# Optimization experiments

Hardware: AMD Instinct MI355X
Metric: run time of the kernel (lower is better)

Reference implementation:

```python
import jax, jax.numpy as jnp
import numpy as np
import math

B = 524288
D = 4
CTX = 64
HID = 128
IN_DIM = 2 + CTX  # keep_idx len is 2 for every mask
# default_masks_D(4, 10) dedups to exactly these 4 masks (torch module therefore has 4 layers)
KEEP = ((0, 1), (1, 2), (2, 3), (0, 3))
TRANS = ((2, 3), (0, 3), (0, 1), (1, 2))
L = 4


def _mlp(x, W1, b1, W2, b2, W3, b3):
    # MLP(in_dim, out_dim, hidden=128, depth=2): Lin+GELU, Lin+GELU, Lin
    x = jax.nn.gelu(x @ W1 + b1, approximate=False)
    x = jax.nn.gelu(x @ W2 + b2, approximate=False)
    return x @ W3 + b3


def setup_inputs() -> dict:
    key = jax.random.key(0)
    ks = jax.random.split(key, 16)
    theta = jax.random.normal(ks[0], (B, D), dtype=jnp.float32)
    h = jax.random.normal(ks[1], (B, CTX), dtype=jnp.float32)
    p = lambda k, shape: jax.random.normal(k, shape, dtype=jnp.float32) * 0.02
    inp = {"theta": theta, "h": h}
    # stacked per-layer weights for s_net and t_net
    for pref, off in (("s", 2), ("t", 8)):
        inp[pref + "W1"] = p(ks[off + 0], (L, IN_DIM, HID))
        inp[pref + "b1"] = p(ks[off + 1], (L, HID))
        inp[pref + "W2"] = p(ks[off + 2], (L, HID, HID))
        inp[pref + "b2"] = p(ks[off + 3], (L, HID))
        inp[pref + "W3"] = p(ks[off + 4], (L, HID, 2))
        inp[pref + "b3"] = p(ks[off + 5], (L, 2))
    return inp


def reference(theta, h, sW1, sb1, sW2, sb2, sW3, sb3, tW1, tb1, tW2, tb2, tW3, tb3):
    # ConditionalRealNVP.log_prob(theta, h)
    x = theta
    logdet = jnp.zeros(theta.shape[0], dtype=theta.dtype)
    for i in range(L):
        keep = np.array(KEEP[i])
        trans = np.array(TRANS[i])
        xp = jnp.concatenate([x[:, keep], h], axis=1)  # [B, 66]
        s = _mlp(xp, sW1[i], sb1[i], sW2[i], sb2[i], sW3[i], sb3[i])  # [B, 2]
        t = _mlp(xp, tW1[i], tb1[i], tW2[i], tb2[i], tW3[i], tb3[i])  # [B, 2]
        x = x.at[:, trans].set(x[:, trans] * jnp.exp(s) + t)
        logdet = logdet + s.sum(axis=1)
    log_pz = -0.5 * (x ** 2).sum(axis=1) - 0.5 * D * math.log(2 * math.pi)
    return log_pz + logdet
```

## Files before the change

kernel.cpp:

```cpp
#include <hip/hip_runtime.h>
#include <hip/hip_bf16.h>

typedef short short8 __attribute__((ext_vector_type(8)));
typedef float f32x4 __attribute__((ext_vector_type(4)));
typedef float f32x2 __attribute__((ext_vector_type(2)));
typedef unsigned short u16;
typedef unsigned int u32;
typedef u32 u32x4 __attribute__((ext_vector_type(4)));

#define NL_STRIDE 57344
#define OFF_W1F 0
#define OFF_W2F 16384
#define OFF_W3F 49152
#define OFF_W1K 53248
#define OFF_B1  54272
#define OFF_B2  54784
#define OFF_B3  55296

__device__ __forceinline__ u16 f2bf(float f) {
  union { float f; unsigned int u; } v; v.f = f;
  unsigned int r = v.u + 0x7fffu + ((v.u >> 16) & 1u);
  return (u16)(r >> 16);
}

__device__ __forceinline__ u32 cvt_pk_bf16(float lo, float hi) {
  u32 r;
  asm("v_cvt_pk_bf16_f32 %0, %1, %2" : "=v"(r) : "v"(lo), "v"(hi));
  return r;
}

__device__ __forceinline__ f32x2 bc2(float s) { return (f32x2){s, s}; }

__device__ __forceinline__ f32x2 gelu2(f32x2 x) {
  f32x2 u = x * x;
  f32x2 t = u * 0.00417617f + (-0.0560330f);
  t = t * u + 0.394326f;
  f32x2 s = x * t + 0.5f;
  s.x = __builtin_amdgcn_fmed3f(s.x, 0.0f, 1.0f);
  s.y = __builtin_amdgcn_fmed3f(s.y, 0.0f, 1.0f);
  return x * s;
}

__device__ __forceinline__ int perm_col(int p) {
  return (p & ~31) | ((p & 1) << 4) | ((p & 31) >> 1);
}

__global__ __launch_bounds__(256) void prep_kernel(
    const float* __restrict__ sW1, const float* __restrict__ sb1,
    const float* __restrict__ sW2, const float* __restrict__ sb2,
    const float* __restrict__ sW3, const float* __restrict__ sb3,
    const float* __restrict__ tW1, const float* __restrict__ tb1,
    const float* __restrict__ tW2, const float* __restrict__ tb2,
    const float* __restrict__ tW3, const float* __restrict__ tb3,
    char* __restrict__ ws)
{
  int nl = blockIdx.x;
  int layer = nl >> 1, net = nl & 1;
  const float* W1 = net ? tW1 : sW1;
  const float* W2 = net ? tW2 : sW2;
  const float* W3 = net ? tW3 : sW3;
  const float* B1 = net ? tb1 : sb1;
  const float* B2 = net ? tb2 : sb2;
  const float* B3 = net ? tb3 : sb3;
  char* base = ws + (size_t)nl * NL_STRIDE;
  int e = blockIdx.y * 256 + (int)threadIdx.x;

  if (e < 8192) {
    int kt = e >> 12, rem = e & 4095, nt = rem >> 9, r2 = rem & 511;
    int l = r2 >> 3, j = r2 & 7;
    int k = kt * 32 + (l >> 4) * 8 + j, n = nt * 16 + (l & 15);
    ((u16*)(base + OFF_W1F))[e] = f2bf(W1[layer * 8448 + (2 + k) * 128 + n]);
  } else if (e < 24576) {
    int e2 = e - 8192;
    int kt = e2 >> 12, nt = (e2 >> 9) & 7, l = (e2 >> 3) & 63, j = e2 & 7;
    int kp = kt * 32 + (l >> 4) * 8 + j, n = nt * 16 + (l & 15);
    int c = perm_col(kp);
    ((u16*)(base + OFF_W2F))[e2] = f2bf(W2[layer * 16384 + c * 128 + n]);
  } else if (e < 26624) {
    int e3 = e - 24576;
    int kt = e3 >> 9, l = (e3 >> 3) & 63, j = e3 & 7;
    int kp = kt * 32 + (l >> 4) * 8 + j, n = l & 15;
    int c = perm_col(kp);
    float v = (n < 2) ? W3[layer * 256 + c * 2 + n] : 0.0f;
    ((u16*)(base + OFF_W3F))[e3] = f2bf(v);
  } else if (e < 26880) {
    int e4 = e - 26624; int r = e4 >> 7, n = e4 & 127;
    ((float*)(base + OFF_W1K))[e4] = W1[layer * 8448 + r * 128 + n];
  } else if (e < 27008) {
    int e5 = e - 26880; ((float*)(base + OFF_B1))[e5] = B1[layer * 128 + e5];
  } else if (e < 27136) {
    int e6 = e - 27008; ((float*)(base + OFF_B2))[e6] = B2[layer * 128 + e6];
  } else if (e < 27138) {
    int e7 = e - 27136; ((float*)(base + OFF_B3))[e7] = B3[layer * 2 + e7];
  }
}

__global__ __launch_bounds__(256, 5) void realnvp_kernel(
    const float* __restrict__ theta, const float* __restrict__ h_g,
    const char* __restrict__ ws, float* __restrict__ out)
{
  __shared__ __align__(16) u16 hs[64 * 64];
  __shared__ __align__(16) u16 hid[64 * 128];
  __shared__ __align__(16) float x_lds[64 * 4];
  __shared__ __align__(8)  float xk_lds[2 * 64];
  __shared__ float sbuf[2 * 64 * 2];

  const int tid = (int)threadIdx.x;
  const int row0 = (int)blockIdx.x * 64;
  const int wv = tid >> 6, lane = tid & 63, q = lane >> 4, lr = lane & 15;
  const char* hsB = (const char*)hs;
  char* hidB = (char*)hid;
  const int swz = (lr & 7) << 4;

  if (tid < 64) {
    float4 t4 = *(const float4*)(theta + (size_t)(row0 + tid) * 4);
    *(f32x4*)&x_lds[tid * 4] = (f32x4){t4.x, t4.y, t4.z, t4.w};
    xk_lds[tid]      = t4.x;
    xk_lds[64 + tid] = t4.y;
  }
  {
    int r = tid >> 2, hf = tid & 3;
    const float* src = h_g + (size_t)(row0 + r) * 64 + hf * 16;
    const int wswz = (r & 7) << 4;
#pragma unroll
    for (int c = 0; c < 16; c += 8) {
      float4 f0 = *(const float4*)(src + c);
      float4 f1 = *(const float4*)(src + c + 4);
      u32x4 o;
      o[0] = cvt_pk_bf16(f0.x, f0.y);
      o[1] = cvt_pk_bf16(f0.z, f0.w);
      o[2] = cvt_pk_bf16(f1.x, f1.y);
      o[3] = cvt_pk_bf16(f1.z, f1.w);
      *(u32x4*)((char*)hs + (((r * 64 + hf * 16 + c) * 2) ^ wswz)) = o;
    }
  }
  __syncthreads();

  float logdet = 0.0f;
  const f32x4 zero4 = {0.f, 0.f, 0.f, 0.f};
  const int col0 = wv * 32 + lr;

  unsigned wb[4];
#pragma unroll
  for (int r = 0; r < 4; ++r) {
    int rl = q * 4 + r;
    wb[r] = (unsigned)((rl * 256 + wv * 64 + lr * 4) ^ ((rl & 7) << 4));
  }

#pragma unroll 1
  for (int layer = 0; layer < 4; ++layer) {
#pragma unroll 1
    for (int net = 0; net < 2; ++net) {
      const char* base = ws + (size_t)(layer * 2 + net) * NL_STRIDE;
      const u16* w1f = (const u16*)(base + OFF_W1F);
      const u16* w2f = (const u16*)(base + OFF_W2F);
      const u16* w3f = (const u16*)(base + OFF_W3F);
      const float* w1k = (const float*)(base + OFF_W1K);
      const float* b1 = (const float*)(base + OFF_B1);
      const float* b2 = (const float*)(base + OFF_B2);
      const float* b3 = (const float*)(base + OFF_B3);

      f32x4 acc[4][2];
#pragma unroll
      for (int mt = 0; mt < 4; ++mt) { acc[mt][0] = zero4; acc[mt][1] = zero4; }
      __builtin_amdgcn_s_setprio(1);
#pragma unroll
      for (int kt = 0; kt < 2; ++kt) {
        const int abase = (((lr * 64 + kt * 32 + q * 8) * 2)) ^ swz;
        short8 a[4];
#pragma unroll
        for (int mt = 0; mt < 4; ++mt)
          a[mt] = *(const short8*)(hsB + abase + mt * 2048);
        short8 b0 = *(const short8*)(w1f + (kt * 8 + wv * 2 + 0) * 512 + lane * 8);
        short8 b1v = *(const short8*)(w1f + (kt * 8 + wv * 2 + 1) * 512 + lane * 8);
#pragma unroll
        for (int mt = 0; mt < 4; ++mt) {
          acc[mt][0] = __builtin_amdgcn_mfma_f32_16x16x32_bf16(a[mt], b0, acc[mt][0], 0, 0, 0);
          acc[mt][1] = __builtin_amdgcn_mfma_f32_16x16x32_bf16(a[mt], b1v, acc[mt][1], 0, 0, 0);
        }
      }
      __builtin_amdgcn_s_setprio(0);
      float wk00 = w1k[col0],       wk01 = w1k[col0 + 16];
      float wk10 = w1k[128 + col0], wk11 = w1k[128 + col0 + 16];
      float bb0 = b1[col0], bb1 = b1[col0 + 16];
      __syncthreads();
#pragma unroll
      for (int mt = 0; mt < 4; ++mt) {
        int rb = mt * 16 + q * 4;
#pragma unroll
        for (int p = 0; p < 2; ++p) {
          int row = rb + 2 * p;
          f32x2 xk0 = *(const f32x2*)(xk_lds + row);
          f32x2 xk1 = *(const f32x2*)(xk_lds + 64 + row);
          f32x2 vA = {acc[mt][0][2 * p], acc[mt][0][2 * p + 1]};
          f32x2 vB = {acc[mt][1][2 * p], acc[mt][1][2 * p + 1]};
          vA = vA + bc2(bb0); vA = xk0 * bc2(wk00) + vA; vA = xk1 * bc2(wk10) + vA;
          vB = vB + bc2(bb1); vB = xk0 * bc2(wk01) + vB; vB = xk1 * bc2(wk11) + vB;
          f32x2 gA = gelu2(vA), gB = gelu2(vB);
          *(u32*)(hidB + (wb[2 * p]     + mt * 4096)) = cvt_pk_bf16(gA.x, gB.x);
          *(u32*)(hidB + (wb[2 * p + 1] + mt * 4096)) = cvt_pk_bf16(gA.y, gB.y);
        }
      }
      __syncthreads();

      f32x4 acc2[4][2];
#pragma unroll
      for (int mt = 0; mt < 4; ++mt) { acc2[mt][0] = zero4; acc2[mt][1] = zero4; }
      __builtin_amdgcn_s_setprio(1);
#pragma unroll
      for (int kt = 0; kt < 4; ++kt) {
        const int abase = ((lr * 256 + kt * 64 + q * 16)) ^ swz;
        short8 a[4];
#pragma unroll
        for (int mt = 0; mt < 4; ++mt)
          a[mt] = *(const short8*)(hidB + abase + mt * 4096);
        short8 b0 = *(const short8*)(w2f + (kt * 8 + wv * 2 + 0) * 512 + lane * 8);
        short8 b1v = *(const short8*)(w2f + (kt * 8 + wv * 2 + 1) * 512 + lane * 8);
#pragma unroll
        for (int mt = 0; mt < 4; ++mt) {
          acc2[mt][0] = __builtin_amdgcn_mfma_f32_16x16x32_bf16(a[mt], b0, acc2[mt][0], 0, 0, 0);
          acc2[mt][1] = __builtin_amdgcn_mfma_f32_16x16x32_bf16(a[mt], b1v, acc2[mt][1], 0, 0, 0);
        }
      }
      __builtin_amdgcn_s_setprio(0);
      float cb0 = b2[col0], cb1 = b2[col0 + 16];
      __syncthreads();
#pragma unroll
      for (int mt = 0; mt < 4; ++mt) {
#pragma unroll
        for (int p = 0; p < 2; ++p) {
          f32x2 vA = {acc2[mt][0][2 * p], acc2[mt][0][2 * p + 1]};
          f32x2 vB = {acc2[mt][1][2 * p], acc2[mt][1][2 * p + 1]};
          vA = vA + bc2(cb0);
          vB = vB + bc2(cb1);
          f32x2 gA = gelu2(vA), gB = gelu2(vB);
          *(u32*)(hidB + (wb[2 * p]     + mt * 4096)) = cvt_pk_bf16(gA.x, gB.x);
          *(u32*)(hidB + (wb[2 * p + 1] + mt * 4096)) = cvt_pk_bf16(gA.y, gB.y);
        }
      }
      __syncthreads();

      f32x4 acc3 = zero4;
#pragma unroll
      for (int kt = 0; kt < 4; ++kt) {
        short8 b = *(const short8*)(w3f + kt * 512 + lane * 8);
        const int abase = ((lr * 256 + kt * 64 + q * 16)) ^ swz;
        short8 a = *(const short8*)(hidB + abase + wv * 4096);
        acc3 = __builtin_amdgcn_mfma_f32_16x16x32_bf16(a, b, acc3, 0, 0, 0);
      }
      if (lr < 2) {
        float bbv = b3[lr];
        int rb = wv * 16 + q * 4;
#pragma unroll
        for (int r = 0; r < 4; ++r)
          sbuf[net * 128 + (rb + r) * 2 + lr] = acc3[r] + bbv;
      }
      __syncthreads();
    }

    if (tid < 64) {
      float s0 = sbuf[tid * 2 + 0], s1 = sbuf[tid * 2 + 1];
      float t0 = sbuf[128 + tid * 2 + 0], t1 = sbuf[128 + tid * 2 + 1];
      int a0 = (0x1002 >> (layer * 4)) & 15;
      int a1 = (0x2133 >> (layer * 4)) & 15;
      x_lds[tid * 4 + a0] = x_lds[tid * 4 + a0] * __expf(s0) + t0;
      x_lds[tid * 4 + a1] = x_lds[tid * 4 + a1] * __expf(s1) + t1;
      logdet += s0 + s1;
      int nl_ = (layer + 1) & 3;
      int nk0 = (0x0210 >> (nl_ * 4)) & 15;
      int nk1 = (0x3321 >> (nl_ * 4)) & 15;
      xk_lds[tid]      = x_lds[tid * 4 + nk0];
      xk_lds[64 + tid] = x_lds[tid * 4 + nk1];
    }
    __syncthreads();
  }

  if (tid < 64) {
    float x0 = x_lds[tid * 4 + 0], x1 = x_lds[tid * 4 + 1];
    float x2 = x_lds[tid * 4 + 2], x3 = x_lds[tid * 4 + 3];
    out[row0 + tid] = -0.5f * (x0 * x0 + x1 * x1 + x2 * x2 + x3 * x3)
                      - 3.6757541328f + logdet;
  }
}

extern "C" void kernel_launch(void* const* d_in, const int* in_sizes, int n_in,
                              void* d_out, int out_size, void* d_ws, size_t ws_size,
                              hipStream_t stream) {
  (void)in_sizes; (void)n_in; (void)out_size; (void)ws_size;
  const float* theta = (const float*)d_in[0];
  const float* h     = (const float*)d_in[1];
  const float* sW1 = (const float*)d_in[2],  *sb1 = (const float*)d_in[3];
  const float* sW2 = (const float*)d_in[4],  *sb2 = (const float*)d_in[5];
  const float* sW3 = (const float*)d_in[6],  *sb3 = (const float*)d_in[7];
  const float* tW1 = (const float*)d_in[8],  *tb1 = (const float*)d_in[9];
  const float* tW2 = (const float*)d_in[10], *tb2 = (const float*)d_in[11];
  const float* tW3 = (const float*)d_in[12], *tb3 = (const float*)d_in[13];
  float* out = (float*)d_out;
  char* ws = (char*)d_ws;

  dim3 pgrid(8, 107);
  prep_kernel<<<pgrid, 256, 0, stream>>>(sW1, sb1, sW2, sb2, sW3, sb3,
                                         tW1, tb1, tW2, tb2, tW3, tb3, ws);
  realnvp_kernel<<<8192, 256, 0, stream>>>(theta, h, (const char*)ws, out);
}
```

Before: 526.7 us.

## Run s and t networks concurrently with 512-thread blocks and per-net hidden buffers

Doubles the block to 512 threads so waves 0-3 evaluate the s-net and waves 4-7 the t-net at the same time, each with its own hidden-activation LDS buffer. The net loop disappears, which halves the number of serialized layer phases and barriers per block. The h staging load is respread over 512 threads. In exchange, LDS use per block grows, register pressure rises under the launch bound of 512 threads with min 6 blocks, and fewer blocks may be resident per CU.

Measured after the change: 621.8 us. 1.18x slower.

```diff
diff --git a/kernel.cpp b/kernel.cpp
--- a/kernel.cpp
+++ b/kernel.cpp
@@ -95,12 +95,12 @@
   }
 }
 
-__global__ __launch_bounds__(256, 5) void realnvp_kernel(
+__global__ __launch_bounds__(512, 6) void realnvp_kernel(
     const float* __restrict__ theta, const float* __restrict__ h_g,
     const char* __restrict__ ws, float* __restrict__ out)
 {
   __shared__ __align__(16) u16 hs[64 * 64];
-  __shared__ __align__(16) u16 hid[64 * 128];
+  __shared__ __align__(16) u16 hid[2][64 * 128];
   __shared__ __align__(16) float x_lds[64 * 4];
   __shared__ __align__(8)  float xk_lds[2 * 64];
   __shared__ float sbuf[2 * 64 * 2];
@@ -108,8 +108,10 @@
   const int tid = (int)threadIdx.x;
   const int row0 = (int)blockIdx.x * 64;
   const int wv = tid >> 6, lane = tid & 63, q = lane >> 4, lr = lane & 15;
+  const int sn = wv >> 2;
+  const int wq = wv & 3;
   const char* hsB = (const char*)hs;
-  char* hidB = (char*)hid;
+  char* hidB = (char*)hid[sn];
   const int swz = (lr & 7) << 4;
 
   if (tid < 64) {
@@ -119,144 +121,138 @@
     xk_lds[64 + tid] = t4.y;
   }
   {
-    int r = tid >> 2, hf = tid & 3;
-    const float* src = h_g + (size_t)(row0 + r) * 64 + hf * 16;
-    const int wswz = (r & 7) << 4;
-#pragma unroll
-    for (int c = 0; c < 16; c += 8) {
-      float4 f0 = *(const float4*)(src + c);
-      float4 f1 = *(const float4*)(src + c + 4);
-      u32x4 o;
-      o[0] = cvt_pk_bf16(f0.x, f0.y);
-      o[1] = cvt_pk_bf16(f0.z, f0.w);
-      o[2] = cvt_pk_bf16(f1.x, f1.y);
-      o[3] = cvt_pk_bf16(f1.z, f1.w);
-      *(u32x4*)((char*)hs + (((r * 64 + hf * 16 + c) * 2) ^ wswz)) = o;
-    }
+    int r = tid >> 3, hf = tid & 7;
+    const float* src = h_g + (size_t)(row0 + r) * 64 + hf * 8;
+    float4 f0 = *(const float4*)(src);
+    float4 f1 = *(const float4*)(src + 4);
+    u32x4 o;
+    o[0] = cvt_pk_bf16(f0.x, f0.y);
+    o[1] = cvt_pk_bf16(f0.z, f0.w);
+    o[2] = cvt_pk_bf16(f1.x, f1.y);
+    o[3] = cvt_pk_bf16(f1.z, f1.w);
+    *(u32x4*)((char*)hs + (((r * 64 + hf * 8) * 2) ^ ((r & 7) << 4))) = o;
   }
   __syncthreads();
 
   float logdet = 0.0f;
   const f32x4 zero4 = {0.f, 0.f, 0.f, 0.f};
-  const int col0 = wv * 32 + lr;
+  const int col0 = wq * 32 + lr;
 
   unsigned wb[4];
 #pragma unroll
   for (int r = 0; r < 4; ++r) {
     int rl = q * 4 + r;
-    wb[r] = (unsigned)((rl * 256 + wv * 64 + lr * 4) ^ ((rl & 7) << 4));
+    wb[r] = (unsigned)((rl * 256 + wq * 64 + lr * 4) ^ ((rl & 7) << 4));
   }
 
 #pragma unroll 1
   for (int layer = 0; layer < 4; ++layer) {
-#pragma unroll 1
-    for (int net = 0; net < 2; ++net) {
-      const char* base = ws + (size_t)(layer * 2 + net) * NL_STRIDE;
-      const u16* w1f = (const u16*)(base + OFF_W1F);
-      const u16* w2f = (const u16*)(base + OFF_W2F);
-      const u16* w3f = (const u16*)(base + OFF_W3F);
-      const float* w1k = (const float*)(base + OFF_W1K);
-      const float* b1 = (const float*)(base + OFF_B1);
-      const float* b2 = (const float*)(base + OFF_B2);
-      const float* b3 = (const float*)(base + OFF_B3);
-
-      f32x4 acc[4][2];
-#pragma unroll
-      for (int mt = 0; mt < 4; ++mt) { acc[mt][0] = zero4; acc[mt][1] = zero4; }
-      __builtin_amdgcn_s_setprio(1);
-#pragma unroll
-      for (int kt = 0; kt < 2; ++kt) {
-        const int abase = (((lr * 64 + kt * 32 + q * 8) * 2)) ^ swz;
-        short8 a[4];
-#pragma unroll
-        for (int mt = 0; mt < 4; ++mt)
-          a[mt] = *(const short8*)(hsB + abase + mt * 2048);
-        short8 b0 = *(const short8*)(w1f + (kt * 8 + wv * 2 + 0) * 512 + lane * 8);
-        short8 b1v = *(const short8*)(w1f + (kt * 8 + wv * 2 + 1) * 512 + lane * 8);
-#pragma unroll
-        for (int mt = 0; mt < 4; ++mt) {
-          acc[mt][0] = __builtin_amdgcn_mfma_f32_16x16x32_bf16(a[mt], b0, acc[mt][0], 0, 0, 0);
-          acc[mt][1] = __builtin_amdgcn_mfma_f32_16x16x32_bf16(a[mt], b1v, acc[mt][1], 0, 0, 0);
-        }
-      }
-      __builtin_amdgcn_s_setprio(0);
-      float wk00 = w1k[col0],       wk01 = w1k[col0 + 16];
-      float wk10 = w1k[128 + col0], wk11 = w1k[128 + col0 + 16];
-      float bb0 = b1[col0], bb1 = b1[col0 + 16];
-      __syncthreads();
+    const char* base = ws + (size_t)(layer * 2 + sn) * NL_STRIDE;
+    const u16* w1f = (const u16*)(base + OFF_W1F);
+    const u16* w2f = (const u16*)(base + OFF_W2F);
+    const u16* w3f = (const u16*)(base + OFF_W3F);
+    const float* w1k = (const float*)(base + OFF_W1K);
+    const float* b1 = (const float*)(base + OFF_B1);
+    const float* b2 = (const float*)(base + OFF_B2);
+    const float* b3 = (const float*)(base + OFF_B3);
+
+    f32x4 acc[4][2];
+#pragma unroll
+    for (int mt = 0; mt < 4; ++mt) { acc[mt][0] = zero4; acc[mt][1] = zero4; }
+    __builtin_amdgcn_s_setprio(1);
+#pragma unroll
+    for (int kt = 0; kt < 2; ++kt) {
+      const int abase = (((lr * 64 + kt * 32 + q * 8) * 2)) ^ swz;
+      short8 a[4];
+#pragma unroll
+      for (int mt = 0; mt < 4; ++mt)
+        a[mt] = *(const short8*)(hsB + abase + mt * 2048);
+      short8 b0 = *(const short8*)(w1f + (kt * 8 + wq * 2 + 0) * 512 + lane * 8);
+      short8 b1v = *(const short8*)(w1f + (kt * 8 + wq * 2 + 1) * 512 + lane * 8);
 #pragma unroll
       for (int mt = 0; mt < 4; ++mt) {
-        int rb = mt * 16 + q * 4;
-#pragma unroll
-        for (int p = 0; p < 2; ++p) {
-          int row = rb + 2 * p;
-          f32x2 xk0 = *(const f32x2*)(xk_lds + row);
-          f32x2 xk1 = *(const f32x2*)(xk_lds + 64 + row);
-          f32x2 vA = {acc[mt][0][2 * p], acc[mt][0][2 * p + 1]};
-          f32x2 vB = {acc[mt][1][2 * p], acc[mt][1][2 * p + 1]};
-          vA = vA + bc2(bb0); vA = xk0 * bc2(wk00) + vA; vA = xk1 * bc2(wk10) + vA;
-          vB = vB + bc2(bb1); vB = xk0 * bc2(wk01) + vB; vB = xk1 * bc2(wk11) + vB;
-          f32x2 gA = gelu2(vA), gB = gelu2(vB);
-          *(u32*)(hidB + (wb[2 * p]     + mt * 4096)) = cvt_pk_bf16(gA.x, gB.x);
-          *(u32*)(hidB + (wb[2 * p + 1] + mt * 4096)) = cvt_pk_bf16(gA.y, gB.y);
-        }
-      }
-      __syncthreads();
-
-      f32x4 acc2[4][2];
-#pragma unroll
-      for (int mt = 0; mt < 4; ++mt) { acc2[mt][0] = zero4; acc2[mt][1] = zero4; }
-      __builtin_amdgcn_s_setprio(1);
-#pragma unroll
-      for (int kt = 0; kt < 4; ++kt) {
-        const int abase = ((lr * 256 + kt * 64 + q * 16)) ^ swz;
-        short8 a[4];
-#pragma unroll
-        for (int mt = 0; mt < 4; ++mt)
-          a[mt] = *(const short8*)(hidB + abase + mt * 4096);
-        short8 b0 = *(const short8*)(w2f + (kt * 8 + wv * 2 + 0) * 512 + lane * 8);
-        short8 b1v = *(const short8*)(w2f + (kt * 8 + wv * 2 + 1) * 512 + lane * 8);
-#pragma unroll
-        for (int mt = 0; mt < 4; ++mt) {
-          acc2[mt][0] = __builtin_amdgcn_mfma_f32_16x16x32_bf16(a[mt], b0, acc2[mt][0], 0, 0, 0);
-          acc2[mt][1] = __builtin_amdgcn_mfma_f32_16x16x32_bf16(a[mt], b1v, acc2[mt][1], 0, 0, 0);
-        }
-      }
-      __builtin_amdgcn_s_setprio(0);
-      float cb0 = b2[col0], cb1 = b2[col0 + 16];
-      __syncthreads();
+        acc[mt][0] = __builtin_amdgcn_mfma_f32_16x16x32_bf16(a[mt], b0, acc[mt][0], 0, 0, 0);
+        acc[mt][1] = __builtin_amdgcn_mfma_f32_16x16x32_bf16(a[mt], b1v, acc[mt][1], 0, 0, 0);
+      }
+    }
+    __builtin_amdgcn_s_setprio(0);
+    float wk00 = w1k[col0],       wk01 = w1k[col0 + 16];
+    float wk10 = w1k[128 + col0], wk11 = w1k[128 + col0 + 16];
+    float bb0 = b1[col0], bb1 = b1[col0 + 16];
+#pragma unroll
+    for (int mt = 0; mt < 4; ++mt) {
+      int rb = mt * 16 + q * 4;
+#pragma unroll
+      for (int p = 0; p < 2; ++p) {
+        int row = rb + 2 * p;
+        f32x2 xk0 = *(const f32x2*)(xk_lds + row);
+        f32x2 xk1 = *(const f32x2*)(xk_lds + 64 + row);
+        f32x2 vA = {acc[mt][0][2 * p], acc[mt][0][2 * p + 1]};
+        f32x2 vB = {acc[mt][1][2 * p], acc[mt][1][2 * p + 1]};
+        vA = vA + bc2(bb0); vA = xk0 * bc2(wk00) + vA; vA = xk1 * bc2(wk10) + vA;
+        vB = vB + bc2(bb1); vB = xk0 * bc2(wk01) + vB; vB = xk1 * bc2(wk11) + vB;
+        f32x2 gA = gelu2(vA), gB = gelu2(vB);
+        *(u32*)(hidB + (wb[2 * p]     + mt * 4096)) = cvt_pk_bf16(gA.x, gB.x);
+        *(u32*)(hidB + (wb[2 * p + 1] + mt * 4096)) = cvt_pk_bf16(gA.y, gB.y);
+      }
+    }
+    __syncthreads();
+
+    f32x4 acc2[4][2];
+#pragma unroll
+    for (int mt = 0; mt < 4; ++mt) { acc2[mt][0] = zero4; acc2[mt][1] = zero4; }
+    __builtin_amdgcn_s_setprio(1);
+#pragma unroll
+    for (int kt = 0; kt < 4; ++kt) {
+      const int abase = ((lr * 256 + kt * 64 + q * 16)) ^ swz;
+      short8 a[4];
+#pragma unroll
+      for (int mt = 0; mt < 4; ++mt)
+        a[mt] = *(const short8*)(hidB + abase + mt * 4096);
+      short8 b0 = *(const short8*)(w2f + (kt * 8 + wq * 2 + 0) * 512 + lane * 8);
+      short8 b1v = *(const short8*)(w2f + (kt * 8 + wq * 2 + 1) * 512 + lane * 8);
 #pragma unroll
       for (int mt = 0; mt < 4; ++mt) {
-#pragma unroll
-        for (int p = 0; p < 2; ++p) {
-          f32x2 vA = {acc2[mt][0][2 * p], acc2[mt][0][2 * p + 1]};
-          f32x2 vB = {acc2[mt][1][2 * p], acc2[mt][1][2 * p + 1]};
-          vA = vA + bc2(cb0);
-          vB = vB + bc2(cb1);
-          f32x2 gA = gelu2(vA), gB = gelu2(vB);
-          *(u32*)(hidB + (wb[2 * p]     + mt * 4096)) = cvt_pk_bf16(gA.x, gB.x);
-          *(u32*)(hidB + (wb[2 * p + 1] + mt * 4096)) = cvt_pk_bf16(gA.y, gB.y);
-        }
-      }
-      __syncthreads();
-
+        acc2[mt][0] = __builtin_amdgcn_mfma_f32_16x16x32_bf16(a[mt], b0, acc2[mt][0], 0, 0, 0);
+        acc2[mt][1] = __builtin_amdgcn_mfma_f32_16x16x32_bf16(a[mt], b1v, acc2[mt][1], 0, 0, 0);
+      }
+    }
+    __builtin_amdgcn_s_setprio(0);
+    float cb0 = b2[col0], cb1 = b2[col0 + 16];
+    __syncthreads();
+#pragma unroll
+    for (int mt = 0; mt < 4; ++mt) {
+#pragma unroll
+      for (int p = 0; p < 2; ++p) {
+        f32x2 vA = {acc2[mt][0][2 * p], acc2[mt][0][2 * p + 1]};
+        f32x2 vB = {acc2[mt][1][2 * p], acc2[mt][1][2 * p + 1]};
+        vA = vA + bc2(cb0);
+        vB = vB + bc2(cb1);
+        f32x2 gA = gelu2(vA), gB = gelu2(vB);
+        *(u32*)(hidB + (wb[2 * p]     + mt * 4096)) = cvt_pk_bf16(gA.x, gB.x);
+        *(u32*)(hidB + (wb[2 * p + 1] + mt * 4096)) = cvt_pk_bf16(gA.y, gB.y);
+      }
+    }
+    __syncthreads();
+
+    {
       f32x4 acc3 = zero4;
 #pragma unroll
       for (int kt = 0; kt < 4; ++kt) {
         short8 b = *(const short8*)(w3f + kt * 512 + lane * 8);
         const int abase = ((lr * 256 + kt * 64 + q * 16)) ^ swz;
-        short8 a = *(const short8*)(hidB + abase + wv * 4096);
+        short8 a = *(const short8*)(hidB + abase + wq * 4096);
         acc3 = __builtin_amdgcn_mfma_f32_16x16x32_bf16(a, b, acc3, 0, 0, 0);
       }
       if (lr < 2) {
         float bbv = b3[lr];
-        int rb = wv * 16 + q * 4;
+        int rb = wq * 16 + q * 4;
 #pragma unroll
         for (int r = 0; r < 4; ++r)
-          sbuf[net * 128 + (rb + r) * 2 + lr] = acc3[r] + bbv;
-      }
-      __syncthreads();
-    }
+          sbuf[sn * 128 + (rb + r) * 2 + lr] = acc3[r] + bbv;
+      }
+    }
+    __syncthreads();
 
     if (tid < 64) {
       float s0 = sbuf[tid * 2 + 0], s1 = sbuf[tid * 2 + 1];
@@ -301,5 +297,5 @@
   dim3 pgrid(8, 107);
   prep_kernel<<<pgrid, 256, 0, stream>>>(sW1, sb1, sW2, sb2, sW3, sb3,
                                          tW1, tb1, tW2, tb2, tW3, tb3, ws);
-  realnvp_kernel<<<8192, 256, 0, stream>>>(theta, h, (const char*)ws, out);
-}
+  realnvp_kernel<<<8192, 512, 0, stream>>>(theta, h, (const char*)ws, out);
+}
```

## Retile MLP GEMMs to 2x2 wave grid over rows and columns

Applied to the files above, without the earlier changes.

Changes the per-wave work split from all 64 rows by 32 columns to 32 rows by 64 columns (two M-halves by two N-halves), with the column permutation in the weight prep and the hidden-layer store layout updated to match. Each wave now loads 2 A fragments and 4 B fragments per k-step instead of 4 A and 2 B, which cuts LDS reads of activations and raises global/L2 reads of weight fragments. The risk is more weight-fetch pressure and a more complex layout mapping that has to stay consistent between the prep kernel and the main kernel.

After: 987.8 us. +87.6%, slower.

```diff
diff --git a/kernel.cpp b/kernel.cpp
--- a/kernel.cpp
+++ b/kernel.cpp
@@ -42,7 +42,7 @@
 }
 
 __device__ __forceinline__ int perm_col(int p) {
-  return (p & ~31) | ((p & 1) << 4) | ((p & 31) >> 1);
+  return (p & ~63) | (((p >> 5) & 1) << 5) | ((p & 1) << 4) | ((p >> 1) & 15);
 }
 
 __global__ __launch_bounds__(256) void prep_kernel(
@@ -108,6 +108,8 @@
   const int tid = (int)threadIdx.x;
   const int row0 = (int)blockIdx.x * 64;
   const int wv = tid >> 6, lane = tid & 63, q = lane >> 4, lr = lane & 15;
+  const int mhalf = wv >> 1;
+  const int nq = wv & 1;
   const char* hsB = (const char*)hs;
   char* hidB = (char*)hid;
   const int swz = (lr & 7) << 4;
@@ -138,13 +140,13 @@
 
   float logdet = 0.0f;
   const f32x4 zero4 = {0.f, 0.f, 0.f, 0.f};
-  const int col0 = wv * 32 + lr;
+  const int col0 = nq * 64 + lr;
 
   unsigned wb[4];
 #pragma unroll
   for (int r = 0; r < 4; ++r) {
     int rl = q * 4 + r;
-    wb[r] = (unsigned)((rl * 256 + wv * 64 + lr * 4) ^ ((rl & 7) << 4));
+    wb[r] = (unsigned)((rl * 256 + nq * 128 + lr * 4) ^ ((rl & 7) << 4));
   }
 
 #pragma unroll 1
@@ -160,82 +162,116 @@
       const float* b2 = (const float*)(base + OFF_B2);
       const float* b3 = (const float*)(base + OFF_B3);
 
-      f32x4 acc[4][2];
-#pragma unroll
-      for (int mt = 0; mt < 4; ++mt) { acc[mt][0] = zero4; acc[mt][1] = zero4; }
+      f32x4 acc[2][4];
+#pragma unroll
+      for (int mt = 0; mt < 2; ++mt)
+#pragma unroll
+        for (int nt = 0; nt < 4; ++nt) acc[mt][nt] = zero4;
       __builtin_amdgcn_s_setprio(1);
 #pragma unroll
       for (int kt = 0; kt < 2; ++kt) {
         const int abase = (((lr * 64 + kt * 32 + q * 8) * 2)) ^ swz;
-        short8 a[4];
-#pragma unroll
-        for (int mt = 0; mt < 4; ++mt)
-          a[mt] = *(const short8*)(hsB + abase + mt * 2048);
-        short8 b0 = *(const short8*)(w1f + (kt * 8 + wv * 2 + 0) * 512 + lane * 8);
-        short8 b1v = *(const short8*)(w1f + (kt * 8 + wv * 2 + 1) * 512 + lane * 8);
-#pragma unroll
-        for (int mt = 0; mt < 4; ++mt) {
-          acc[mt][0] = __builtin_amdgcn_mfma_f32_16x16x32_bf16(a[mt], b0, acc[mt][0], 0, 0, 0);
-          acc[mt][1] = __builtin_amdgcn_mfma_f32_16x16x32_bf16(a[mt], b1v, acc[mt][1], 0, 0, 0);
+        short8 a0 = *(const short8*)(hsB + abase + (mhalf * 2 + 0) * 2048);
+        short8 a1 = *(const short8*)(hsB + abase + (mhalf * 2 + 1) * 2048);
+        short8 b[4];
+#pragma unroll
+        for (int nt = 0; nt < 4; ++nt)
+          b[nt] = *(const short8*)(w1f + (kt * 8 + nq * 4 + nt) * 512 + lane * 8);
+#pragma unroll
+        for (int nt = 0; nt < 4; ++nt) {
+          acc[0][nt] = __builtin_amdgcn_mfma_f32_16x16x32_bf16(a0, b[nt], acc[0][nt], 0, 0, 0);
+          acc[1][nt] = __builtin_amdgcn_mfma_f32_16x16x32_bf16(a1, b[nt], acc[1][nt], 0, 0, 0);
         }
       }
       __builtin_amdgcn_s_setprio(0);
-      float wk00 = w1k[col0],       wk01 = w1k[col0 + 16];
-      float wk10 = w1k[128 + col0], wk11 = w1k[128 + col0 + 16];
-      float bb0 = b1[col0], bb1 = b1[col0 + 16];
-      __syncthreads();
-#pragma unroll
-      for (int mt = 0; mt < 4; ++mt) {
-        int rb = mt * 16 + q * 4;
+      float wk0[4], wk1[4], bb[4];
+#pragma unroll
+      for (int i = 0; i < 4; ++i) {
+        wk0[i] = w1k[col0 + i * 16];
+        wk1[i] = w1k[128 + col0 + i * 16];
+        bb[i]  = b1[col0 + i * 16];
+      }
+      __syncthreads();
+#pragma unroll
+      for (int mt = 0; mt < 2; ++mt) {
+        const int moff = (mhalf * 2 + mt) * 4096;
+        const int rbase = mhalf * 32 + mt * 16 + q * 4;
 #pragma unroll
         for (int p = 0; p < 2; ++p) {
-          int row = rb + 2 * p;
+          int row = rbase + 2 * p;
           f32x2 xk0 = *(const f32x2*)(xk_lds + row);
           f32x2 xk1 = *(const f32x2*)(xk_lds + 64 + row);
-          f32x2 vA = {acc[mt][0][2 * p], acc[mt][0][2 * p + 1]};
-          f32x2 vB = {acc[mt][1][2 * p], acc[mt][1][2 * p + 1]};
-          vA = vA + bc2(bb0); vA = xk0 * bc2(wk00) + vA; vA = xk1 * bc2(wk10) + vA;
-          vB = vB + bc2(bb1); vB = xk0 * bc2(wk01) + vB; vB = xk1 * bc2(wk11) + vB;
-          f32x2 gA = gelu2(vA), gB = gelu2(vB);
-          *(u32*)(hidB + (wb[2 * p]     + mt * 4096)) = cvt_pk_bf16(gA.x, gB.x);
-          *(u32*)(hidB + (wb[2 * p + 1] + mt * 4096)) = cvt_pk_bf16(gA.y, gB.y);
+          f32x2 g0, g1, g2, g3;
+          {
+            f32x2 v0 = {acc[mt][0][2 * p], acc[mt][0][2 * p + 1]};
+            v0 = v0 + bc2(bb[0]); v0 = xk0 * bc2(wk0[0]) + v0; v0 = xk1 * bc2(wk1[0]) + v0;
+            g0 = gelu2(v0);
+            f32x2 v1 = {acc[mt][1][2 * p], acc[mt][1][2 * p + 1]};
+            v1 = v1 + bc2(bb[1]); v1 = xk0 * bc2(wk0[1]) + v1; v1 = xk1 * bc2(wk1[1]) + v1;
+            g1 = gelu2(v1);
+            f32x2 v2 = {acc[mt][2][2 * p], acc[mt][2][2 * p + 1]};
+            v2 = v2 + bc2(bb[2]); v2 = xk0 * bc2(wk0[2]) + v2; v2 = xk1 * bc2(wk1[2]) + v2;
+            g2 = gelu2(v2);
+            f32x2 v3 = {acc[mt][3][2 * p], acc[mt][3][2 * p + 1]};
+            v3 = v3 + bc2(bb[3]); v3 = xk0 * bc2(wk0[3]) + v3; v3 = xk1 * bc2(wk1[3]) + v3;
+            g3 = gelu2(v3);
+          }
+          unsigned w0 = wb[2 * p] + moff, w1 = wb[2 * p + 1] + moff;
+          *(u32*)(hidB + w0) = cvt_pk_bf16(g0.x, g1.x);
+          *(u32*)(hidB + w1) = cvt_pk_bf16(g0.y, g1.y);
+          *(u32*)(hidB + (w0 ^ 64)) = cvt_pk_bf16(g2.x, g3.x);
+          *(u32*)(hidB + (w1 ^ 64)) = cvt_pk_bf16(g2.y, g3.y);
         }
       }
       __syncthreads();
 
-      f32x4 acc2[4][2];
-#pragma unroll
-      for (int mt = 0; mt < 4; ++mt) { acc2[mt][0] = zero4; acc2[mt][1] = zero4; }
+      f32x4 acc2[2][4];
+#pragma unroll
+      for (int mt = 0; mt < 2; ++mt)
+#pragma unroll
+        for (int nt = 0; nt < 4; ++nt) acc2[mt][nt] = zero4;
       __builtin_amdgcn_s_setprio(1);
 #pragma unroll
       for (int kt = 0; kt < 4; ++kt) {
         const int abase = ((lr * 256 + kt * 64 + q * 16)) ^ swz;
-        short8 a[4];
-#pragma unroll
-        for (int mt = 0; mt < 4; ++mt)
-          a[mt] = *(const short8*)(hidB + abase + mt * 4096);
-        short8 b0 = *(const short8*)(w2f + (kt * 8 + wv * 2 + 0) * 512 + lane * 8);
-        short8 b1v = *(const short8*)(w2f + (kt * 8 + wv * 2 + 1) * 512 + lane * 8);
-#pragma unroll
-        for (int mt = 0; mt < 4; ++mt) {
-          acc2[mt][0] = __builtin_amdgcn_mfma_f32_16x16x32_bf16(a[mt], b0, acc2[mt][0], 0, 0, 0);
-          acc2[mt][1] = __builtin_amdgcn_mfma_f32_16x16x32_bf16(a[mt], b1v, acc2[mt][1], 0, 0, 0);
+        short8 a0 = *(const short8*)(hidB + abase + (mhalf * 2 + 0) * 4096);
+        short8 a1 = *(const short8*)(hidB + abase + (mhalf * 2 + 1) * 4096);
+        short8 b[4];
+#pragma unroll
+        for (int nt = 0; nt < 4; ++nt)
+          b[nt] = *(const short8*)(w2f + (kt * 8 + nq * 4 + nt) * 512 + lane * 8);
+#pragma unroll
+        for (int nt = 0; nt < 4; ++nt) {
+          acc2[0][nt] = __builtin_amdgcn_mfma_f32_16x16x32_bf16(a0, b[nt], acc2[0][nt], 0, 0, 0);
+          acc2[1][nt] = __builtin_amdgcn_mfma_f32_16x16x32_bf16(a1, b[nt], acc2[1][nt], 0, 0, 0);
         }
       }
       __builtin_amdgcn_s_setprio(0);
-      float cb0 = b2[col0], cb1 = b2[col0 + 16];
-      __syncthreads();
-#pragma unroll
-      for (int mt = 0; mt < 4; ++mt) {
+      float cb[4];
+#pragma unroll
+      for (int i = 0; i < 4; ++i) cb[i] = b2[col0 + i * 16];
+      __syncthreads();
+#pragma unroll
+      for (int mt = 0; mt < 2; ++mt) {
+        const int moff = (mhalf * 2 + mt) * 4096;
 #pragma unroll
         for (int p = 0; p < 2; ++p) {
-          f32x2 vA = {acc2[mt][0][2 * p], acc2[mt][0][2 * p + 1]};
-          f32x2 vB = {acc2[mt][1][2 * p], acc2[mt][1][2 * p + 1]};
-          vA = vA + bc2(cb0);
-          vB = vB + bc2(cb1);
-          f32x2 gA = gelu2(vA), gB = gelu2(vB);
-          *(u32*)(hidB + (wb[2 * p]     + mt * 4096)) = cvt_pk_bf16(gA.x, gB.x);
-          *(u32*)(hidB + (wb[2 * p + 1] + mt * 4096)) = cvt_pk_bf16(gA.y, gB.y);
+          f32x2 g0, g1, g2, g3;
+          {
+            f32x2 v0 = {acc2[mt][0][2 * p], acc2[mt][0][2 * p + 1]};
+            g0 = gelu2(v0 + bc2(cb[0]));
+            f32x2 v1 = {acc2[mt][1][2 * p], acc2[mt][1][2 * p + 1]};
+            g1 = gelu2(v1 + bc2(cb[1]));
+            f32x2 v2 = {acc2[mt][2][2 * p], acc2[mt][2][2 * p + 1]};
+            g2 = gelu2(v2 + bc2(cb[2]));
+            f32x2 v3 = {acc2[mt][3][2 * p], acc2[mt][3][2 * p + 1]};
+            g3 = gelu2(v3 + bc2(cb[3]));
+          }
+          unsigned w0 = wb[2 * p] + moff, w1 = wb[2 * p + 1] + moff;
+          *(u32*)(hidB + w0) = cvt_pk_bf16(g0.x, g1.x);
+          *(u32*)(hidB + w1) = cvt_pk_bf16(g0.y, g1.y);
+          *(u32*)(hidB + (w0 ^ 64)) = cvt_pk_bf16(g2.x, g3.x);
+          *(u32*)(hidB + (w1 ^ 64)) = cvt_pk_bf16(g2.y, g3.y);
         }
       }
       __syncthreads();
```
